# Performance work log

Measured on AMD Instinct MI355X. Metric: run time of the kernel, lower is better.

## Reference

```python
import jax, jax.numpy as jnp
import numpy as np

B, IN_F, OUT_F, KD = 256, 1024, 128, 16


def setup_inputs() -> dict:
    key = jax.random.key(0)
    k1, k2 = jax.random.split(key)
    x = jax.random.normal(k1, (B, IN_F), dtype=jnp.float32)
    t_mat = jax.random.normal(k2, (IN_F, OUT_F, KD), dtype=jnp.float32)
    return {"x": x, "t_mat": t_mat}


def reference(x, t_mat):
    # Projection: [B, in] @ [in, out*kd] -> [B, out, kd]
    m = jnp.einsum('bi,iok->bok', x, t_mat)
    # All-pairs L1 distance over kernel dim: [B, B, out]
    norm = jnp.sum(jnp.abs(m[:, None, :, :] - m[None, :, :, :]), axis=-1)
    # exp(-norm) summed over the partner axis; subtract 1 for self-pair (norm=0 -> exp=1)
    o_b = jnp.sum(jnp.exp(-norm), axis=1) - 1.0  # [B, out]
    return jnp.concatenate([x, o_b], axis=1)  # [B, in + out]
```

## Files before the change

kernel.cpp:

```cpp
#include <hip/hip_runtime.h>
#include <hip/hip_fp16.h>


#define BATCH 256
#define INF   1024
#define OUTF  128
#define KDIM  16
#define TCOLS 2048
#define OCOLS 1152
#define XB    1032
#define PMW   12

typedef __attribute__((ext_vector_type(8))) short short8;
typedef __attribute__((ext_vector_type(4))) float f32x4;
typedef __attribute__((ext_vector_type(4))) unsigned short ushort4v;

__device__ inline unsigned short bf_trunc(float f) {
    return (unsigned short)(__float_as_uint(f) >> 16);
}

__global__ __launch_bounds__(256) void k_prep(const float* __restrict__ x,
                                              unsigned short* __restrict__ xs,
                                              float* __restrict__ out) {
    const int b = blockIdx.x, t = threadIdx.x;
    const int i = b * 256 + t;
    float4 v = reinterpret_cast<const float4*>(x)[i];
    ushort4v o4 = { bf_trunc(v.x), bf_trunc(v.y), bf_trunc(v.z), bf_trunc(v.w) };
    reinterpret_cast<ushort4v*>(xs)[i] = o4;
    reinterpret_cast<float4*>(out)[b * 288 + t] = v;
}

__global__ __launch_bounds__(256, 2) void k_gemm(const float* __restrict__ T,
                                                 const unsigned short* __restrict__ xs,
                                                 __half* __restrict__ mh) {
    const int blk = blockIdx.x;
    const int o   = blk & 127;
    const int mq  = blk >> 7;
    const int tid = threadIdx.x;
    const int wave = tid >> 6, lane = tid & 63;
    const int l15 = lane & 15, q = lane >> 4;

    __shared__ unsigned short bs[16][XB];
    __shared__ __half pmout[64][16];

    const int mt = mq * 4 + wave;
    const unsigned short* xr = xs + (mt * 16 + l15) * INF + q * 8;

    short8 a[16];
    #pragma unroll
    for (int i = 0; i < 16; ++i)
        a[i] = *reinterpret_cast<const short8*>(xr + i * 32);
    __builtin_amdgcn_sched_barrier(0);

    {
        const int kb = tid >> 2, n0 = (tid & 3) * 4;
        #pragma unroll
        for (int g = 0; g < 4; ++g) {
            float4 tv[4];
            #pragma unroll
            for (int p = 0; p < 4; ++p)
                tv[p] = *reinterpret_cast<const float4*>(
                    &T[((g * 4 + p) * 64 + kb) * TCOLS + o * KDIM + n0]);
            #pragma unroll
            for (int p = 0; p < 4; ++p) {
                const int k = (g * 4 + p) * 64 + kb;
                bs[n0 + 0][k] = bf_trunc(tv[p].x);
                bs[n0 + 1][k] = bf_trunc(tv[p].y);
                bs[n0 + 2][k] = bf_trunc(tv[p].z);
                bs[n0 + 3][k] = bf_trunc(tv[p].w);
            }
        }
    }
    __syncthreads();

    f32x4 acc = {0.f, 0.f, 0.f, 0.f};
    #pragma unroll
    for (int ks = 0; ks < 16; ++ks) {
        short8 bfr = *reinterpret_cast<const short8*>(&bs[l15][ks * 32 + q * 8]);
        acc = __builtin_amdgcn_mfma_f32_16x16x32_bf16(a[ks], bfr, acc, 0, 0, 0);
    }
    #pragma unroll
    for (int i = 0; i < 16; ++i)
        a[i] = *reinterpret_cast<const short8*>(xr + (16 + i) * 32);
    __builtin_amdgcn_sched_barrier(0);
    #pragma unroll
    for (int ks = 0; ks < 16; ++ks) {
        short8 bfr = *reinterpret_cast<const short8*>(&bs[l15][(16 + ks) * 32 + q * 8]);
        acc = __builtin_amdgcn_mfma_f32_16x16x32_bf16(a[ks], bfr, acc, 0, 0, 0);
    }

    #pragma unroll
    for (int r = 0; r < 4; ++r)
        pmout[wave * 16 + q * 4 + r][l15] = __float2half(acc[r]);
    __syncthreads();

    if (tid < 128) {
        const int row = tid >> 1, hh = tid & 1;
        uint4 v = *reinterpret_cast<const uint4*>(&pmout[row][hh * 8]);
        *reinterpret_cast<uint4*>(&mh[o * (BATCH * KDIM) + (mq * 64 + row) * KDIM + hh * 8]) = v;
    }
}

__global__ __launch_bounds__(1024, 4) void k_pair(const __half* __restrict__ mh,
                                                  float* __restrict__ out) {
    const int blk = blockIdx.x;
    const int o   = blk & 127;
    const int h   = blk >> 7;
    const int tid = threadIdx.x;

    __shared__ __half2 pm[BATCH][PMW];
    __shared__ float part[32][128];

    if (tid < 512) {
        uint4 v = *reinterpret_cast<const uint4*>(
            &mh[o * (BATCH * KDIM) + (tid >> 1) * KDIM + (tid & 1) * 8]);
        *reinterpret_cast<uint4*>(&pm[tid >> 1][(tid & 1) * 4]) = v;
    }
    __syncthreads();

    const int i1 = tid & 31;
    const int bsel = tid >> 5;
    __half2 my[4][8];
    #pragma unroll
    for (int r = 0; r < 4; ++r) {
        union { uint4 u[2]; __half2 hh[8]; } c;
        c.u[0] = *reinterpret_cast<const uint4*>(&pm[h * 128 + r * 32 + i1][0]);
        c.u[1] = *reinterpret_cast<const uint4*>(&pm[h * 128 + r * 32 + i1][4]);
        #pragma unroll
        for (int j = 0; j < 8; ++j) my[r][j] = c.hh[j];
    }

    union U16 { uint4 u[2]; __half2 hh[8]; };
    float tot[4] = {0.f, 0.f, 0.f, 0.f};
    const int b2_lo = bsel * 8;

    U16 c0, c1;
    c0.u[0] = *reinterpret_cast<const uint4*>(&pm[b2_lo][0]);
    c0.u[1] = *reinterpret_cast<const uint4*>(&pm[b2_lo][4]);

    #pragma unroll
    for (int ib = 0; ib < 8; ib += 2) {
        c1.u[0] = *reinterpret_cast<const uint4*>(&pm[b2_lo + ib + 1][0]);
        c1.u[1] = *reinterpret_cast<const uint4*>(&pm[b2_lo + ib + 1][4]);
        #pragma unroll
        for (int r = 0; r < 4; ++r) {
            __half2 e0 = __habs2(__hsub2(my[r][0], c0.hh[0]));
            __half2 e1 = __habs2(__hsub2(my[r][1], c0.hh[1]));
            __half2 e2 = __habs2(__hsub2(my[r][2], c0.hh[2]));
            __half2 e3 = __habs2(__hsub2(my[r][3], c0.hh[3]));
            e0 = __hadd2(e0, __habs2(__hsub2(my[r][4], c0.hh[4])));
            e1 = __hadd2(e1, __habs2(__hsub2(my[r][5], c0.hh[5])));
            e2 = __hadd2(e2, __habs2(__hsub2(my[r][6], c0.hh[6])));
            e3 = __hadd2(e3, __habs2(__hsub2(my[r][7], c0.hh[7])));
            __half2 es = __hadd2(__hadd2(e0, e1), __hadd2(e2, e3));
            float n = __low2float(es) + __high2float(es);
            tot[r] += __expf(-n);
        }
        if (ib + 2 < 8) {
            c0.u[0] = *reinterpret_cast<const uint4*>(&pm[b2_lo + ib + 2][0]);
            c0.u[1] = *reinterpret_cast<const uint4*>(&pm[b2_lo + ib + 2][4]);
        }
        #pragma unroll
        for (int r = 0; r < 4; ++r) {
            __half2 e0 = __habs2(__hsub2(my[r][0], c1.hh[0]));
            __half2 e1 = __habs2(__hsub2(my[r][1], c1.hh[1]));
            __half2 e2 = __habs2(__hsub2(my[r][2], c1.hh[2]));
            __half2 e3 = __habs2(__hsub2(my[r][3], c1.hh[3]));
            e0 = __hadd2(e0, __habs2(__hsub2(my[r][4], c1.hh[4])));
            e1 = __hadd2(e1, __habs2(__hsub2(my[r][5], c1.hh[5])));
            e2 = __hadd2(e2, __habs2(__hsub2(my[r][6], c1.hh[6])));
            e3 = __hadd2(e3, __habs2(__hsub2(my[r][7], c1.hh[7])));
            __half2 es = __hadd2(__hadd2(e0, e1), __hadd2(e2, e3));
            float n = __low2float(es) + __high2float(es);
            tot[r] += __expf(-n);
        }
    }
    #pragma unroll
    for (int r = 0; r < 4; ++r)
        part[bsel][r * 32 + i1] = tot[r];
    __syncthreads();

    {
        const int g = tid >> 7, b1 = tid & 127;
        float s = part[g * 4 + 0][b1] + part[g * 4 + 1][b1]
                + part[g * 4 + 2][b1] + part[g * 4 + 3][b1];
        __syncthreads();
        part[g * 4][b1] = s;
    }
    __syncthreads();
    if (tid < 128) {
        float s = -1.0f;
        #pragma unroll
        for (int g = 0; g < 8; ++g) s += part[g * 4][tid];
        out[(h * 128 + tid) * OCOLS + INF + o] = s;
    }
}

extern "C" void kernel_launch(void* const* d_in, const int* in_sizes, int n_in,
                              void* d_out, int out_size, void* d_ws, size_t ws_size,
                              hipStream_t stream) {
    const float* x = (const float*)d_in[0];
    const float* T = (const float*)d_in[1];
    float* out = (float*)d_out;
    unsigned short* xs = (unsigned short*)d_ws;
    __half* mh = (__half*)((char*)d_ws + (1u << 20));

    k_prep<<<256, 256, 0, stream>>>(x, xs, out);
    k_gemm<<<512, 256, 0, stream>>>(T, xs, mh);
    k_pair<<<256, 1024, 0, stream>>>(mh, out);
}
```

Measured before the change: 83.06 us.

## Fuse prep, GEMM and pairwise kernels into one grid-synchronized kernel

```diff
diff --git a/kernel.cpp b/kernel.cpp
--- a/kernel.cpp
+++ b/kernel.cpp
@@ -10,111 +10,129 @@
 #define OCOLS 1152
 #define XB    1032
 #define PMW   12
+#define NBLK  256
 
 typedef __attribute__((ext_vector_type(8))) short short8;
 typedef __attribute__((ext_vector_type(4))) float f32x4;
-typedef __attribute__((ext_vector_type(4))) unsigned short ushort4v;
-
+
+__device__ inline unsigned pack_bf2(float lo, float hi) {
+    return __builtin_amdgcn_perm(__float_as_uint(hi), __float_as_uint(lo), 0x07060302u);
+}
 __device__ inline unsigned short bf_trunc(float f) {
     return (unsigned short)(__float_as_uint(f) >> 16);
 }
 
-__global__ __launch_bounds__(256) void k_prep(const float* __restrict__ x,
-                                              unsigned short* __restrict__ xs,
-                                              float* __restrict__ out) {
-    const int b = blockIdx.x, t = threadIdx.x;
-    const int i = b * 256 + t;
-    float4 v = reinterpret_cast<const float4*>(x)[i];
-    ushort4v o4 = { bf_trunc(v.x), bf_trunc(v.y), bf_trunc(v.z), bf_trunc(v.w) };
-    reinterpret_cast<ushort4v*>(xs)[i] = o4;
-    reinterpret_cast<float4*>(out)[b * 288 + t] = v;
-}
-
-__global__ __launch_bounds__(256, 2) void k_gemm(const float* __restrict__ T,
-                                                 const unsigned short* __restrict__ xs,
-                                                 __half* __restrict__ mh) {
-    const int blk = blockIdx.x;
-    const int o   = blk & 127;
-    const int mq  = blk >> 7;
-    const int tid = threadIdx.x;
-    const int wave = tid >> 6, lane = tid & 63;
-    const int l15 = lane & 15, q = lane >> 4;
-
-    __shared__ unsigned short bs[16][XB];
-    __shared__ __half pmout[64][16];
-
-    const int mt = mq * 4 + wave;
-    const unsigned short* xr = xs + (mt * 16 + l15) * INF + q * 8;
-
-    short8 a[16];
-    #pragma unroll
-    for (int i = 0; i < 16; ++i)
-        a[i] = *reinterpret_cast<const short8*>(xr + i * 32);
-    __builtin_amdgcn_sched_barrier(0);
-
-    {
-        const int kb = tid >> 2, n0 = (tid & 3) * 4;
-        #pragma unroll
-        for (int g = 0; g < 4; ++g) {
-            float4 tv[4];
-            #pragma unroll
-            for (int p = 0; p < 4; ++p)
-                tv[p] = *reinterpret_cast<const float4*>(
-                    &T[((g * 4 + p) * 64 + kb) * TCOLS + o * KDIM + n0]);
-            #pragma unroll
-            for (int p = 0; p < 4; ++p) {
-                const int k = (g * 4 + p) * 64 + kb;
-                bs[n0 + 0][k] = bf_trunc(tv[p].x);
-                bs[n0 + 1][k] = bf_trunc(tv[p].y);
-                bs[n0 + 2][k] = bf_trunc(tv[p].z);
-                bs[n0 + 3][k] = bf_trunc(tv[p].w);
-            }
-        }
-    }
-    __syncthreads();
-
-    f32x4 acc = {0.f, 0.f, 0.f, 0.f};
-    #pragma unroll
-    for (int ks = 0; ks < 16; ++ks) {
-        short8 bfr = *reinterpret_cast<const short8*>(&bs[l15][ks * 32 + q * 8]);
-        acc = __builtin_amdgcn_mfma_f32_16x16x32_bf16(a[ks], bfr, acc, 0, 0, 0);
-    }
-    #pragma unroll
-    for (int i = 0; i < 16; ++i)
-        a[i] = *reinterpret_cast<const short8*>(xr + (16 + i) * 32);
-    __builtin_amdgcn_sched_barrier(0);
-    #pragma unroll
-    for (int ks = 0; ks < 16; ++ks) {
-        short8 bfr = *reinterpret_cast<const short8*>(&bs[l15][(16 + ks) * 32 + q * 8]);
-        acc = __builtin_amdgcn_mfma_f32_16x16x32_bf16(a[ks], bfr, acc, 0, 0, 0);
-    }
-
-    #pragma unroll
-    for (int r = 0; r < 4; ++r)
-        pmout[wave * 16 + q * 4 + r][l15] = __float2half(acc[r]);
-    __syncthreads();
-
-    if (tid < 128) {
-        const int row = tid >> 1, hh = tid & 1;
-        uint4 v = *reinterpret_cast<const uint4*>(&pmout[row][hh * 8]);
-        *reinterpret_cast<uint4*>(&mh[o * (BATCH * KDIM) + (mq * 64 + row) * KDIM + hh * 8]) = v;
-    }
-}
-
-__global__ __launch_bounds__(1024, 4) void k_pair(const __half* __restrict__ mh,
-                                                  float* __restrict__ out) {
+__global__ __launch_bounds__(1024, 4) void k_all(const float* __restrict__ x,
+                                                 const float* __restrict__ T,
+                                                 __half* __restrict__ mg,
+                                                 unsigned* __restrict__ bar,
+                                                 float* __restrict__ out) {
     const int blk = blockIdx.x;
     const int o   = blk & 127;
     const int h   = blk >> 7;
     const int tid = threadIdx.x;
-
+    const int wave = tid >> 6, lane = tid & 63;
+    const int l15 = lane & 15, q = lane >> 4;
+
+    __shared__ unsigned short bs[16][XB];
     __shared__ __half2 pm[BATCH][PMW];
     __shared__ float part[32][128];
 
-    if (tid < 512) {
+    const int tw = wave >> 1, kh = wave & 1;
+    const float4* xw4 = reinterpret_cast<const float4*>(
+        x + (h * 128 + tw * 16 + l15) * INF + kh * 512 + q * 8);
+    float4 fa[16];
+    #pragma unroll
+    for (int f = 0; f < 8; ++f) { fa[2*f] = xw4[f*8]; fa[2*f+1] = xw4[f*8+1]; }
+    __builtin_amdgcn_sched_barrier(0);
+
+    if (tid < 256)
+        reinterpret_cast<float4*>(out)[blk * 288 + tid] =
+            reinterpret_cast<const float4*>(x)[blk * 256 + tid];
+    {
+        const int kb = tid >> 2, n0 = (tid & 3) * 4;
+        float4 tv[4];
+        #pragma unroll
+        for (int p = 0; p < 4; ++p)
+            tv[p] = *reinterpret_cast<const float4*>(
+                &T[(p * 256 + kb) * TCOLS + o * KDIM + n0]);
+        #pragma unroll
+        for (int p = 0; p < 4; ++p) {
+            const int k = p * 256 + kb;
+            bs[n0 + 0][k] = bf_trunc(tv[p].x);
+            bs[n0 + 1][k] = bf_trunc(tv[p].y);
+            bs[n0 + 2][k] = bf_trunc(tv[p].z);
+            bs[n0 + 3][k] = bf_trunc(tv[p].w);
+        }
+    }
+    __syncthreads();
+
+    f32x4 acc = {0.f, 0.f, 0.f, 0.f};
+    #pragma unroll
+    for (int f = 0; f < 8; ++f) {
+        union { unsigned u[4]; short8 s; } ua;
+        ua.u[0] = pack_bf2(fa[2*f].x,   fa[2*f].y);
+        ua.u[1] = pack_bf2(fa[2*f].z,   fa[2*f].w);
+        ua.u[2] = pack_bf2(fa[2*f+1].x, fa[2*f+1].y);
+        ua.u[3] = pack_bf2(fa[2*f+1].z, fa[2*f+1].w);
+        short8 bfr = *reinterpret_cast<const short8*>(&bs[l15][kh*512 + f*32 + q*8]);
+        acc = __builtin_amdgcn_mfma_f32_16x16x32_bf16(ua.s, bfr, acc, 0, 0, 0);
+    }
+    #pragma unroll
+    for (int f = 0; f < 8; ++f) { fa[2*f] = xw4[(8+f)*8]; fa[2*f+1] = xw4[(8+f)*8+1]; }
+    __builtin_amdgcn_sched_barrier(0);
+    #pragma unroll
+    for (int f = 0; f < 8; ++f) {
+        union { unsigned u[4]; short8 s; } ua;
+        ua.u[0] = pack_bf2(fa[2*f].x,   fa[2*f].y);
+        ua.u[1] = pack_bf2(fa[2*f].z,   fa[2*f].w);
+        ua.u[2] = pack_bf2(fa[2*f+1].x, fa[2*f+1].y);
+        ua.u[3] = pack_bf2(fa[2*f+1].z, fa[2*f+1].w);
+        short8 bfr = *reinterpret_cast<const short8*>(&bs[l15][kh*512 + (8+f)*32 + q*8]);
+        acc = __builtin_amdgcn_mfma_f32_16x16x32_bf16(ua.s, bfr, acc, 0, 0, 0);
+    }
+
+    {
+        float* abuf = &part[0][0];
+        #pragma unroll
+        for (int r = 0; r < 4; ++r) abuf[wave * 256 + lane * 4 + r] = acc[r];
+        __syncthreads();
+        if (kh == 0) {
+            __half* pmh = reinterpret_cast<__half*>(pm);
+            #pragma unroll
+            for (int r = 0; r < 4; ++r) {
+                float s = acc[r] + abuf[(wave + 1) * 256 + lane * 4 + r];
+                pmh[(h * 128 + tw * 16 + q * 4 + r) * (2 * PMW) + l15] = __float2half(s);
+            }
+        }
+    }
+    __syncthreads();
+
+    if (tid < 256) {
+        const int row = tid >> 1, hh = tid & 1;
+        uint4 v = *reinterpret_cast<const uint4*>(&pm[h * 128 + row][hh * 4]);
+        *reinterpret_cast<uint4*>(&mg[(o * BATCH + h * 128 + row) * KDIM + hh * 8]) = v;
+    }
+
+    __threadfence();
+    __syncthreads();
+    if (tid == 0) {
+        __hip_atomic_fetch_add(bar, 1u, __ATOMIC_RELEASE, __HIP_MEMORY_SCOPE_AGENT);
+        unsigned v;
+        do {
+            __builtin_amdgcn_s_sleep(2);
+            v = __hip_atomic_load(bar, __ATOMIC_ACQUIRE, __HIP_MEMORY_SCOPE_AGENT);
+        } while (v < NBLK);
+    }
+    __syncthreads();
+    __threadfence();
+
+    if (tid < 256) {
+        const int row = tid >> 1, hh = tid & 1;
+        const int ph = h ^ 1;
         uint4 v = *reinterpret_cast<const uint4*>(
-            &mh[o * (BATCH * KDIM) + (tid >> 1) * KDIM + (tid & 1) * 8]);
-        *reinterpret_cast<uint4*>(&pm[tid >> 1][(tid & 1) * 4]) = v;
+            &mg[(o * BATCH + ph * 128 + row) * KDIM + hh * 8]);
+        *reinterpret_cast<uint4*>(&pm[ph * 128 + row][hh * 4]) = v;
     }
     __syncthreads();
 
@@ -202,10 +220,9 @@
     const float* x = (const float*)d_in[0];
     const float* T = (const float*)d_in[1];
     float* out = (float*)d_out;
-    unsigned short* xs = (unsigned short*)d_ws;
-    __half* mh = (__half*)((char*)d_ws + (1u << 20));
-
-    k_prep<<<256, 256, 0, stream>>>(x, xs, out);
-    k_gemm<<<512, 256, 0, stream>>>(T, xs, mh);
-    k_pair<<<256, 1024, 0, stream>>>(mh, out);
-}
+    __half* mg = (__half*)d_ws;
+    unsigned* bar = (unsigned*)((char*)d_ws + (1u << 20));
+
+    hipMemsetAsync((void*)bar, 0, 64, stream);
+    k_all<<<256, 1024, 0, stream>>>(x, T, mg, bar, out);
+}
```

Result: slower. 220.4 us (+165.4%).

## Remove prep kernel: convert x to bf16 inside GEMM, copy x in pair kernel

Applied to the files above, without the earlier changes.

```diff
diff --git a/kernel.cpp b/kernel.cpp
--- a/kernel.cpp
+++ b/kernel.cpp
@@ -13,25 +13,16 @@
 
 typedef __attribute__((ext_vector_type(8))) short short8;
 typedef __attribute__((ext_vector_type(4))) float f32x4;
-typedef __attribute__((ext_vector_type(4))) unsigned short ushort4v;
-
+
+__device__ inline unsigned pack_bf2(float lo, float hi) {
+    return __builtin_amdgcn_perm(__float_as_uint(hi), __float_as_uint(lo), 0x07060302u);
+}
 __device__ inline unsigned short bf_trunc(float f) {
     return (unsigned short)(__float_as_uint(f) >> 16);
 }
 
-__global__ __launch_bounds__(256) void k_prep(const float* __restrict__ x,
-                                              unsigned short* __restrict__ xs,
-                                              float* __restrict__ out) {
-    const int b = blockIdx.x, t = threadIdx.x;
-    const int i = b * 256 + t;
-    float4 v = reinterpret_cast<const float4*>(x)[i];
-    ushort4v o4 = { bf_trunc(v.x), bf_trunc(v.y), bf_trunc(v.z), bf_trunc(v.w) };
-    reinterpret_cast<ushort4v*>(xs)[i] = o4;
-    reinterpret_cast<float4*>(out)[b * 288 + t] = v;
-}
-
-__global__ __launch_bounds__(256, 2) void k_gemm(const float* __restrict__ T,
-                                                 const unsigned short* __restrict__ xs,
+__global__ __launch_bounds__(256, 2) void k_gemm(const float* __restrict__ x,
+                                                 const float* __restrict__ T,
                                                  __half* __restrict__ mh) {
     const int blk = blockIdx.x;
     const int o   = blk & 127;
@@ -44,12 +35,14 @@
     __shared__ __half pmout[64][16];
 
     const int mt = mq * 4 + wave;
-    const unsigned short* xr = xs + (mt * 16 + l15) * INF + q * 8;
-
-    short8 a[16];
-    #pragma unroll
-    for (int i = 0; i < 16; ++i)
-        a[i] = *reinterpret_cast<const short8*>(xr + i * 32);
+    const float4* xw4 = reinterpret_cast<const float4*>(
+        x + (mt * 16 + l15) * INF + q * 8);
+
+    float4 fa[16], fb[16];
+    #pragma unroll
+    for (int f = 0; f < 8; ++f) { fa[2*f] = xw4[f*8];     fa[2*f+1] = xw4[f*8+1]; }
+    #pragma unroll
+    for (int f = 0; f < 8; ++f) { fb[2*f] = xw4[(8+f)*8]; fb[2*f+1] = xw4[(8+f)*8+1]; }
     __builtin_amdgcn_sched_barrier(0);
 
     {
@@ -75,18 +68,49 @@
 
     f32x4 acc = {0.f, 0.f, 0.f, 0.f};
     #pragma unroll
-    for (int ks = 0; ks < 16; ++ks) {
-        short8 bfr = *reinterpret_cast<const short8*>(&bs[l15][ks * 32 + q * 8]);
-        acc = __builtin_amdgcn_mfma_f32_16x16x32_bf16(a[ks], bfr, acc, 0, 0, 0);
-    }
-    #pragma unroll
-    for (int i = 0; i < 16; ++i)
-        a[i] = *reinterpret_cast<const short8*>(xr + (16 + i) * 32);
+    for (int f = 0; f < 8; ++f) {
+        union { unsigned u[4]; short8 s; } ua;
+        ua.u[0] = pack_bf2(fa[2*f].x,   fa[2*f].y);
+        ua.u[1] = pack_bf2(fa[2*f].z,   fa[2*f].w);
+        ua.u[2] = pack_bf2(fa[2*f+1].x, fa[2*f+1].y);
+        ua.u[3] = pack_bf2(fa[2*f+1].z, fa[2*f+1].w);
+        short8 bfr = *reinterpret_cast<const short8*>(&bs[l15][f * 32 + q * 8]);
+        acc = __builtin_amdgcn_mfma_f32_16x16x32_bf16(ua.s, bfr, acc, 0, 0, 0);
+    }
+    #pragma unroll
+    for (int f = 0; f < 8; ++f) { fa[2*f] = xw4[(16+f)*8]; fa[2*f+1] = xw4[(16+f)*8+1]; }
+    #pragma unroll
+    for (int f = 0; f < 8; ++f) {
+        union { unsigned u[4]; short8 s; } ua;
+        ua.u[0] = pack_bf2(fb[2*f].x,   fb[2*f].y);
+        ua.u[1] = pack_bf2(fb[2*f].z,   fb[2*f].w);
+        ua.u[2] = pack_bf2(fb[2*f+1].x, fb[2*f+1].y);
+        ua.u[3] = pack_bf2(fb[2*f+1].z, fb[2*f+1].w);
+        short8 bfr = *reinterpret_cast<const short8*>(&bs[l15][(8+f) * 32 + q * 8]);
+        acc = __builtin_amdgcn_mfma_f32_16x16x32_bf16(ua.s, bfr, acc, 0, 0, 0);
+    }
+    #pragma unroll
+    for (int f = 0; f < 8; ++f) { fb[2*f] = xw4[(24+f)*8]; fb[2*f+1] = xw4[(24+f)*8+1]; }
     __builtin_amdgcn_sched_barrier(0);
     #pragma unroll
-    for (int ks = 0; ks < 16; ++ks) {
-        short8 bfr = *reinterpret_cast<const short8*>(&bs[l15][(16 + ks) * 32 + q * 8]);
-        acc = __builtin_amdgcn_mfma_f32_16x16x32_bf16(a[ks], bfr, acc, 0, 0, 0);
+    for (int f = 0; f < 8; ++f) {
+        union { unsigned u[4]; short8 s; } ua;
+        ua.u[0] = pack_bf2(fa[2*f].x,   fa[2*f].y);
+        ua.u[1] = pack_bf2(fa[2*f].z,   fa[2*f].w);
+        ua.u[2] = pack_bf2(fa[2*f+1].x, fa[2*f+1].y);
+        ua.u[3] = pack_bf2(fa[2*f+1].z, fa[2*f+1].w);
+        short8 bfr = *reinterpret_cast<const short8*>(&bs[l15][(16+f) * 32 + q * 8]);
+        acc = __builtin_amdgcn_mfma_f32_16x16x32_bf16(ua.s, bfr, acc, 0, 0, 0);
+    }
+    #pragma unroll
+    for (int f = 0; f < 8; ++f) {
+        union { unsigned u[4]; short8 s; } ua;
+        ua.u[0] = pack_bf2(fb[2*f].x,   fb[2*f].y);
+        ua.u[1] = pack_bf2(fb[2*f].z,   fb[2*f].w);
+        ua.u[2] = pack_bf2(fb[2*f+1].x, fb[2*f+1].y);
+        ua.u[3] = pack_bf2(fb[2*f+1].z, fb[2*f+1].w);
+        short8 bfr = *reinterpret_cast<const short8*>(&bs[l15][(24+f) * 32 + q * 8]);
+        acc = __builtin_amdgcn_mfma_f32_16x16x32_bf16(ua.s, bfr, acc, 0, 0, 0);
     }
 
     #pragma unroll
@@ -101,7 +125,8 @@
     }
 }
 
-__global__ __launch_bounds__(1024, 4) void k_pair(const __half* __restrict__ mh,
+__global__ __launch_bounds__(1024, 4) void k_pair(const float* __restrict__ x,
+                                                  const __half* __restrict__ mh,
                                                   float* __restrict__ out) {
     const int blk = blockIdx.x;
     const int o   = blk & 127;
@@ -116,6 +141,9 @@
             &mh[o * (BATCH * KDIM) + (tid >> 1) * KDIM + (tid & 1) * 8]);
         *reinterpret_cast<uint4*>(&pm[tid >> 1][(tid & 1) * 4]) = v;
     }
+    if (tid < 256)
+        reinterpret_cast<float4*>(out)[blk * 288 + tid] =
+            reinterpret_cast<const float4*>(x)[blk * 256 + tid];
     __syncthreads();
 
     const int i1 = tid & 31;
@@ -202,10 +230,8 @@
     const float* x = (const float*)d_in[0];
     const float* T = (const float*)d_in[1];
     float* out = (float*)d_out;
-    unsigned short* xs = (unsigned short*)d_ws;
-    __half* mh = (__half*)((char*)d_ws + (1u << 20));
-
-    k_prep<<<256, 256, 0, stream>>>(x, xs, out);
-    k_gemm<<<512, 256, 0, stream>>>(T, xs, mh);
-    k_pair<<<256, 1024, 0, stream>>>(mh, out);
-}
+    __half* mh = (__half*)d_ws;
+
+    k_gemm<<<512, 256, 0, stream>>>(x, T, mh);
+    k_pair<<<256, 1024, 0, stream>>>(x, mh, out);
+}
```

New measurement: 87.41 us. 5.2% more time.

## Pre-swizzle x into MFMA fragment layout and load all A fragments at once

Applied to the files above, without the earlier changes.

```diff
diff --git a/kernel.cpp b/kernel.cpp
--- a/kernel.cpp
+++ b/kernel.cpp
@@ -13,25 +13,41 @@
 
 typedef __attribute__((ext_vector_type(8))) short short8;
 typedef __attribute__((ext_vector_type(4))) float f32x4;
-typedef __attribute__((ext_vector_type(4))) unsigned short ushort4v;
-
+
+__device__ inline unsigned pack_bf2(float lo, float hi) {
+    return __builtin_amdgcn_perm(__float_as_uint(hi), __float_as_uint(lo), 0x07060302u);
+}
 __device__ inline unsigned short bf_trunc(float f) {
     return (unsigned short)(__float_as_uint(f) >> 16);
 }
 
-__global__ __launch_bounds__(256) void k_prep(const float* __restrict__ x,
-                                              unsigned short* __restrict__ xs,
+__global__ __launch_bounds__(512) void k_prep(const float* __restrict__ x,
+                                              unsigned short* __restrict__ xf,
                                               float* __restrict__ out) {
-    const int b = blockIdx.x, t = threadIdx.x;
-    const int i = b * 256 + t;
-    float4 v = reinterpret_cast<const float4*>(x)[i];
-    ushort4v o4 = { bf_trunc(v.x), bf_trunc(v.y), bf_trunc(v.z), bf_trunc(v.w) };
-    reinterpret_cast<ushort4v*>(xs)[i] = o4;
-    reinterpret_cast<float4*>(out)[b * 288 + t] = v;
+    const int t = blockIdx.x * 512 + threadIdx.x;
+    const int mt = t >> 11, ks = (t >> 6) & 31, lane = t & 63;
+    const int l15 = lane & 15, q = lane >> 4;
+
+    const float* src = x + (mt * 16 + l15) * INF + ks * 32 + q * 8;
+    float4 v0 = *reinterpret_cast<const float4*>(src);
+    float4 v1 = *reinterpret_cast<const float4*>(src + 4);
+    union { unsigned u[4]; short8 s; } ua;
+    ua.u[0] = pack_bf2(v0.x, v0.y);
+    ua.u[1] = pack_bf2(v0.z, v0.w);
+    ua.u[2] = pack_bf2(v1.x, v1.y);
+    ua.u[3] = pack_bf2(v1.z, v1.w);
+    reinterpret_cast<short8*>(xf)[t] = ua.s;
+
+    #pragma unroll
+    for (int j = t; j < 65536; j += 32768) {
+        const int r = j >> 8, c = j & 255;
+        reinterpret_cast<float4*>(out)[r * 288 + c] =
+            reinterpret_cast<const float4*>(x)[j];
+    }
 }
 
 __global__ __launch_bounds__(256, 2) void k_gemm(const float* __restrict__ T,
-                                                 const unsigned short* __restrict__ xs,
+                                                 const unsigned short* __restrict__ xf,
                                                  __half* __restrict__ mh) {
     const int blk = blockIdx.x;
     const int o   = blk & 127;
@@ -44,12 +60,11 @@
     __shared__ __half pmout[64][16];
 
     const int mt = mq * 4 + wave;
-    const unsigned short* xr = xs + (mt * 16 + l15) * INF + q * 8;
-
-    short8 a[16];
-    #pragma unroll
-    for (int i = 0; i < 16; ++i)
-        a[i] = *reinterpret_cast<const short8*>(xr + i * 32);
+    const short8* xr = reinterpret_cast<const short8*>(xf) + mt * 2048 + lane;
+
+    short8 a[32];
+    #pragma unroll
+    for (int ks = 0; ks < 32; ++ks) a[ks] = xr[ks * 64];
     __builtin_amdgcn_sched_barrier(0);
 
     {
@@ -75,17 +90,8 @@
 
     f32x4 acc = {0.f, 0.f, 0.f, 0.f};
     #pragma unroll
-    for (int ks = 0; ks < 16; ++ks) {
+    for (int ks = 0; ks < 32; ++ks) {
         short8 bfr = *reinterpret_cast<const short8*>(&bs[l15][ks * 32 + q * 8]);
-        acc = __builtin_amdgcn_mfma_f32_16x16x32_bf16(a[ks], bfr, acc, 0, 0, 0);
-    }
-    #pragma unroll
-    for (int i = 0; i < 16; ++i)
-        a[i] = *reinterpret_cast<const short8*>(xr + (16 + i) * 32);
-    __builtin_amdgcn_sched_barrier(0);
-    #pragma unroll
-    for (int ks = 0; ks < 16; ++ks) {
-        short8 bfr = *reinterpret_cast<const short8*>(&bs[l15][(16 + ks) * 32 + q * 8]);
         acc = __builtin_amdgcn_mfma_f32_16x16x32_bf16(a[ks], bfr, acc, 0, 0, 0);
     }
 
@@ -202,10 +208,10 @@
     const float* x = (const float*)d_in[0];
     const float* T = (const float*)d_in[1];
     float* out = (float*)d_out;
-    unsigned short* xs = (unsigned short*)d_ws;
+    unsigned short* xf = (unsigned short*)d_ws;
     __half* mh = (__half*)((char*)d_ws + (1u << 20));
 
-    k_prep<<<256, 256, 0, stream>>>(x, xs, out);
-    k_gemm<<<512, 256, 0, stream>>>(T, xs, mh);
+    k_prep<<<64, 512, 0, stream>>>(x, xf, out);
+    k_gemm<<<512, 256, 0, stream>>>(T, xf, mh);
     k_pair<<<256, 1024, 0, stream>>>(mh, out);
 }
```

After: 80.02 us. 1.04x faster.
